# Kernel tuning notes

Hardware: AMD Instinct MI355X
Metric: run time of the kernel (lower is better)

The kernel has to match this reference:

```python
import jax, jax.numpy as jnp
import numpy as np

B, Q, C, H, W, CH = 16, 1024, 256, 32, 32, 8  # batch, queries, dim, grid, conv hidden


def setup_inputs() -> dict:
    key = jax.random.key(0)
    ks = jax.random.split(key, 8)
    return {
        "queries": jax.random.normal(ks[0], (B, Q, C), jnp.float32),
        "keys": jax.random.normal(ks[1], (B, H, W, C), jnp.float32),
        "pos": jax.random.randint(ks[2], (B, Q, 2), 0, H, dtype=jnp.int32),
        "rel_bias": jax.random.normal(ks[3], (2 * H - 1, 2 * W - 1), jnp.float32) * 0.02,
        "conv1_weight": jax.random.normal(ks[4], (CH, 1, 3, 3), jnp.float32) * 0.1,
        "conv1_bias": jnp.zeros((CH,), jnp.float32),
        "conv2_weight": jax.random.normal(ks[5], (1, CH, 3, 3), jnp.float32) * 0.1,
        "conv2_bias": jnp.zeros((1,), jnp.float32),
    }


def reference(queries, keys, pos, rel_bias, conv1_weight, conv1_bias, conv2_weight, conv2_bias):
    Bq, Qn, Cd = queries.shape
    _, Hh, Ww, _ = keys.shape
    # fused relative-grid attention scores: [B,Q,H,W]
    scores = jnp.einsum('bqc,bhwc->bqhw', queries, keys) / jnp.sqrt(jnp.float32(Cd))
    dh = jnp.arange(Hh)[None, None, :] - pos[..., 0][..., None] + (Hh - 1)  # [B,Q,H]
    dw = jnp.arange(Ww)[None, None, :] - pos[..., 1][..., None] + (Ww - 1)  # [B,Q,W]
    bias = rel_bias[dh[..., :, None], dw[..., None, :]]                     # [B,Q,H,W]
    attn = jax.nn.softmax((scores + bias).reshape(Bq, Qn, Hh * Ww), axis=-1)
    attn = attn.reshape(Bq, Qn, Hh, Ww)
    # residual conv block on each (1,H,W) attention map
    x = attn.reshape(Bq * Qn, 1, Hh, Ww)
    dn = ('NCHW', 'OIHW', 'NCHW')
    h = jax.lax.conv_general_dilated(x, conv1_weight, (1, 1), 'SAME', dimension_numbers=dn)
    h = jax.nn.relu(h + conv1_bias[None, :, None, None])
    h = jax.lax.conv_general_dilated(h, conv2_weight, (1, 1), 'SAME', dimension_numbers=dn)
    h = h + conv2_bias[None, :, None, None]
    return (x + h).reshape(Bq, Qn, Hh, Ww)
```

## Files before the change

kernel.cpp:

```cpp
#include <hip/hip_runtime.h>

typedef _Float16 h2 __attribute__((ext_vector_type(2)));
typedef _Float16 h8 __attribute__((ext_vector_type(8)));
typedef float f32x4 __attribute__((ext_vector_type(4)));

#define B_  16
#define Q_  1024
#define C_  256
#define HW_ 1024
#define TQA 32
#define NTA 512
#define QLD 264
#define BT  256
#define IPB 4
#define XRB 80
#define XIMGB (34 * XRB)
#define HRB 576

__device__ __forceinline__ h2 u2h(unsigned u) { return __builtin_bit_cast(h2, u); }
__device__ __forceinline__ unsigned h2u(h2 h) { return __builtin_bit_cast(unsigned, h); }

__device__ __forceinline__ float fdot2f(h2 a, h2 b, float c) {
#if __has_builtin(__builtin_amdgcn_fdot2)
    return __builtin_amdgcn_fdot2(a, b, c, false);
#else
    return c + (float)a[0] * (float)b[0] + (float)a[1] * (float)b[1];
#endif
}
__device__ __forceinline__ float dotw(unsigned x, unsigned w, float acc) {
    return fdot2f(u2h(x), u2h(w), acc);
}

__global__ void cvt_keys_f16(const float* __restrict__ src,
                             _Float16* __restrict__ dst, int n8) {
    int i = blockIdx.x * blockDim.x + threadIdx.x;
    if (i >= n8) return;
    const float4* s = (const float4*)src;
    float4 a = s[2 * i], b = s[2 * i + 1];
    h8 v;
    v[0] = (_Float16)a.x; v[1] = (_Float16)a.y; v[2] = (_Float16)a.z; v[3] = (_Float16)a.w;
    v[4] = (_Float16)b.x; v[5] = (_Float16)b.y; v[6] = (_Float16)b.z; v[7] = (_Float16)b.w;
    *(h8*)(dst + (size_t)i * 8) = v;
}

__global__ void pack_weights(const float* __restrict__ w1, const float* __restrict__ b1,
                             const float* __restrict__ w2, const float* __restrict__ b2,
                             unsigned* __restrict__ wpk) {
    int t = threadIdx.x;
    if (t < 24) {
        int ch = t / 3, dy = t - ch * 3;
        h2 v = {(_Float16)w1[ch * 9 + dy * 3 + 0], (_Float16)w1[ch * 9 + dy * 3 + 1]};
        wpk[t] = h2u(v);
    } else if (t < 48) {
        int i = t - 24; int ch = i / 3, dy = i - ch * 3;
        h2 v = {(_Float16)w1[ch * 9 + dy * 3 + 2], (_Float16)0.f};
        wpk[t] = h2u(v);
    } else if (t < 56) {
        wpk[t] = __builtin_bit_cast(unsigned, b1[t - 48]);
    } else if (t < 92) {
        int i = t - 56; int t9 = i >> 2, c2 = i & 3;
        h2 v = {(_Float16)w2[(2 * c2) * 9 + t9], (_Float16)w2[(2 * c2 + 1) * 9 + t9]};
        wpk[t] = h2u(v);
    } else if (t == 92) {
        wpk[t] = __builtin_bit_cast(unsigned, b2[0]);
    }
}

__global__ __launch_bounds__(NTA, 4) void attn_kernel(
    const float* __restrict__ queries, const _Float16* __restrict__ keysh,
    const int* __restrict__ pos, const float* __restrict__ rel_bias,
    _Float16* __restrict__ xmapg)
{
    __shared__ _Float16 q_lds[TQA * QLD];
    __shared__ _Float16 bias_lds[63 * 64];
    __shared__ float red_max[8][TQA];
    __shared__ float red_sum[8][TQA];
    __shared__ int2  pos_lds[TQA];

    const int tid = threadIdx.x;
    const int bid = blockIdx.x;
    const int swz = (bid & 7) * 64 + (bid >> 3);
    const int batch = swz >> 5;
    const int tile  = swz & 31;

    {
        const float4* qsrc = (const float4*)(queries + (size_t)(batch * Q_ + tile * TQA) * C_);
        #pragma unroll
        for (int i = 0; i < 4; ++i) {
            int e4 = i * NTA + tid;
            float4 v = qsrc[e4];
            int row = e4 >> 6, col4 = e4 & 63;
            _Float16* d = &q_lds[row * QLD + col4 * 4];
            d[0] = (_Float16)v.x; d[1] = (_Float16)v.y;
            d[2] = (_Float16)v.z; d[3] = (_Float16)v.w;
        }
        for (int idx = tid; idx < 63 * 63; idx += NTA) {
            int r = idx / 63;
            bias_lds[r * 64 + (idx - r * 63)] = (_Float16)rel_bias[idx];
        }
        if (tid < TQA)
            pos_lds[tid] = ((const int2*)pos)[batch * Q_ + tile * TQA + tid];
    }
    __syncthreads();

    const int lane = tid & 63;
    const int wv   = tid >> 6;
    const int kgrp = (lane >> 4) * 8;
    const int l15  = lane & 15;
    const int rowbase = (lane >> 4) << 2;

    f32x4 acc0[8], acc1[8];
    #pragma unroll
    for (int f = 0; f < 8; ++f) {
        acc0[f] = f32x4{0.f, 0.f, 0.f, 0.f};
        acc1[f] = f32x4{0.f, 0.f, 0.f, 0.f};
    }

    const _Float16* kb = keysh + (size_t)batch * (HW_ * C_)
                       + (size_t)(wv * 128 + l15) * C_ + kgrp;
    #pragma unroll
    for (int ks = 0; ks < 8; ++ks) {
        h8 a0 = *(const h8*)&q_lds[l15 * QLD + ks * 32 + kgrp];
        h8 a1 = *(const h8*)&q_lds[(16 + l15) * QLD + ks * 32 + kgrp];
        #pragma unroll
        for (int f = 0; f < 8; ++f) {
            h8 bfr = *(const h8*)(kb + f * (16 * C_) + ks * 32);
            acc0[f] = __builtin_amdgcn_mfma_f32_16x16x32_f16(a0, bfr, acc0[f], 0, 0, 0);
            acc1[f] = __builtin_amdgcn_mfma_f32_16x16x32_f16(a1, bfr, acc1[f], 0, 0, 0);
        }
    }

    int p0r[2][4], p1r[2][4];
    #pragma unroll
    for (int mt = 0; mt < 2; ++mt)
        #pragma unroll
        for (int r = 0; r < 4; ++r) {
            int2 pp = pos_lds[mt * 16 + rowbase + r];
            p0r[mt][r] = pp.x; p1r[mt][r] = pp.y;
        }

    float mrow[2][4];
    #pragma unroll
    for (int mt = 0; mt < 2; ++mt)
        #pragma unroll
        for (int r = 0; r < 4; ++r) mrow[mt][r] = -3e38f;

    #pragma unroll
    for (int f = 0; f < 8; ++f) {
        int col = wv * 128 + f * 16 + l15;
        int hh = col >> 5, ww = col & 31;
        #pragma unroll
        for (int r = 0; r < 4; ++r) {
            float s0 = acc0[f][r] * 0.0625f
                     + (float)bias_lds[(hh - p0r[0][r] + 31) * 64 + (ww - p1r[0][r] + 31)];
            acc0[f][r] = s0;
            mrow[0][r] = fmaxf(mrow[0][r], s0);
            float s1 = acc1[f][r] * 0.0625f
                     + (float)bias_lds[(hh - p0r[1][r] + 31) * 64 + (ww - p1r[1][r] + 31)];
            acc1[f][r] = s1;
            mrow[1][r] = fmaxf(mrow[1][r], s1);
        }
    }
    #pragma unroll
    for (int mt = 0; mt < 2; ++mt)
        #pragma unroll
        for (int r = 0; r < 4; ++r) {
            float m = mrow[mt][r];
            m = fmaxf(m, __shfl_xor(m, 1, 64));
            m = fmaxf(m, __shfl_xor(m, 2, 64));
            m = fmaxf(m, __shfl_xor(m, 4, 64));
            m = fmaxf(m, __shfl_xor(m, 8, 64));
            mrow[mt][r] = m;
        }
    if (l15 == 0) {
        #pragma unroll
        for (int mt = 0; mt < 2; ++mt)
            #pragma unroll
            for (int r = 0; r < 4; ++r)
                red_max[wv][mt * 16 + rowbase + r] = mrow[mt][r];
    }
    __syncthreads();

    float M4[2][4];
    #pragma unroll
    for (int mt = 0; mt < 2; ++mt)
        #pragma unroll
        for (int r = 0; r < 4; ++r) {
            float m = red_max[0][mt * 16 + rowbase + r];
            #pragma unroll
            for (int w = 1; w < 8; ++w) m = fmaxf(m, red_max[w][mt * 16 + rowbase + r]);
            M4[mt][r] = m;
        }

    float sm[2][4];
    #pragma unroll
    for (int mt = 0; mt < 2; ++mt)
        #pragma unroll
        for (int r = 0; r < 4; ++r) sm[mt][r] = 0.f;
    #pragma unroll
    for (int f = 0; f < 8; ++f) {
        #pragma unroll
        for (int r = 0; r < 4; ++r) {
            float e0 = __expf(acc0[f][r] - M4[0][r]);
            acc0[f][r] = e0; sm[0][r] += e0;
            float e1 = __expf(acc1[f][r] - M4[1][r]);
            acc1[f][r] = e1; sm[1][r] += e1;
        }
    }
    #pragma unroll
    for (int mt = 0; mt < 2; ++mt)
        #pragma unroll
        for (int r = 0; r < 4; ++r) {
            float s = sm[mt][r];
            s += __shfl_xor(s, 1, 64);
            s += __shfl_xor(s, 2, 64);
            s += __shfl_xor(s, 4, 64);
            s += __shfl_xor(s, 8, 64);
            sm[mt][r] = s;
        }
    if (l15 == 0) {
        #pragma unroll
        for (int mt = 0; mt < 2; ++mt)
            #pragma unroll
            for (int r = 0; r < 4; ++r)
                red_sum[wv][mt * 16 + rowbase + r] = sm[mt][r];
    }
    __syncthreads();

    float sinv[2][4];
    #pragma unroll
    for (int mt = 0; mt < 2; ++mt)
        #pragma unroll
        for (int r = 0; r < 4; ++r) {
            float S = red_sum[0][mt * 16 + rowbase + r];
            #pragma unroll
            for (int w = 1; w < 8; ++w) S += red_sum[w][mt * 16 + rowbase + r];
            sinv[mt][r] = 1.0f / S;
        }

    _Float16* xg = xmapg + (size_t)(batch * Q_ + tile * TQA) * HW_;
    #pragma unroll
    for (int f = 0; f < 8; ++f) {
        int col = wv * 128 + f * 16 + l15;
        #pragma unroll
        for (int r = 0; r < 4; ++r) {
            xg[(size_t)(rowbase + r) * HW_ + col] = (_Float16)(acc0[f][r] * sinv[0][r]);
            xg[(size_t)(16 + rowbase + r) * HW_ + col] = (_Float16)(acc1[f][r] * sinv[1][r]);
        }
    }
}

__global__ __launch_bounds__(BT, 4) void conv_kernel(
    const _Float16* __restrict__ xmapg, const unsigned* __restrict__ wpk,
    float* __restrict__ out)
{
    __shared__ __align__(16) char xall[16 + IPB * XIMGB];
    __shared__ __align__(16) char Hb[34 * HRB];
    __shared__ unsigned wsh[56];

    const int tid = threadIdx.x;
    const int bid = blockIdx.x;
    const int swz = (bid & 7) * 512 + (bid >> 3);
    const size_t img0 = (size_t)swz * IPB;

    {
        const uint4 z = uint4{0u, 0u, 0u, 0u};
        uint4* xz = (uint4*)xall;
        for (int i = tid; i < (int)sizeof(xall) / 16; i += BT) xz[i] = z;
        uint4* hz = (uint4*)Hb;
        for (int i = tid; i < (int)sizeof(Hb) / 16; i += BT) hz[i] = z;
    }
    if (tid < 56) wsh[tid] = wpk[tid];
    __syncthreads();

    #pragma unroll
    for (int i = 0; i < 2; ++i) {
        int c = i * BT + tid;
        int im = c >> 7, cc = c & 127, r = cc >> 2, q = cc & 3;
        uint4 v = *(const uint4*)(xmapg + img0 * HW_ + (size_t)im * HW_ + cc * 8);
        *(uint4*)(xall + 16 + im * XIMGB + (r + 1) * XRB + q * 16) = v;
    }

    unsigned wA[8][3], wB[8][3];
    float b1r[8];
    #pragma unroll
    for (int ch = 0; ch < 8; ++ch) {
        b1r[ch] = __builtin_bit_cast(float, wsh[48 + ch]);
        #pragma unroll
        for (int dy = 0; dy < 3; ++dy) {
            wA[ch][dy] = wsh[ch * 3 + dy];
            wB[ch][dy] = wsh[24 + ch * 3 + dy];
        }
    }
    unsigned w2s[9][4];
    #pragma unroll
    for (int t = 0; t < 9; ++t)
        #pragma unroll
        for (int c2 = 0; c2 < 4; ++c2) w2s[t][c2] = wpk[56 + t * 4 + c2];
    const float b2r = __builtin_bit_cast(float, wpk[92]);

    const int m4 = tid & 7;
    const int y  = tid >> 3;
    const int x0 = m4 << 2;

    const char* const xb  = xall + 16 + y * XRB + 2 * x0;
    char* const hwr = Hb + (y + 1) * HRB + m4 * 16;
    const char* const hrd = Hb + y * HRB + m4 * 16;

    __syncthreads();

    #pragma unroll 1
    for (int img = 0; img < IPB; ++img) {
        const char* xi = xb + img * XIMGB;

        unsigned Pm[3], Pc[3], Pe[3], A0[3], A1[3], E4[3];
        #pragma unroll
        for (int dy = 0; dy < 3; ++dy) {
            unsigned pv = *(const unsigned*)(xi + dy * XRB - 4);
            uint2 a01   = *(const uint2*)(xi + dy * XRB);
            unsigned e4 = *(const unsigned*)(xi + dy * XRB + 8);
            A0[dy] = a01.x; A1[dy] = a01.y; E4[dy] = e4;
            Pm[dy] = __builtin_amdgcn_alignbit(a01.x, pv, 16);
            Pc[dy] = __builtin_amdgcn_alignbit(a01.y, a01.x, 16);
            Pe[dy] = __builtin_amdgcn_alignbit(e4, a01.y, 16);
        }

        unsigned hvw[4][4];
        #pragma unroll
        for (int p = 0; p < 4; ++p) {
            const int cA = 2 * p, cB = 2 * p + 1;
            float sA[4], sB[4];
            #pragma unroll
            for (int j = 0; j < 4; ++j) { sA[j] = b1r[cA]; sB[j] = b1r[cB]; }
            #pragma unroll
            for (int dy = 0; dy < 3; ++dy) {
                sA[0] = dotw(Pm[dy], wA[cA][dy], sA[0]);
                sA[0] = dotw(Pc[dy], wB[cA][dy], sA[0]);
                sA[1] = dotw(A0[dy], wA[cA][dy], sA[1]);
                sA[1] = dotw(A1[dy], wB[cA][dy], sA[1]);
                sA[2] = dotw(Pc[dy], wA[cA][dy], sA[2]);
                sA[2] = dotw(Pe[dy], wB[cA][dy], sA[2]);
                sA[3] = dotw(A1[dy], wA[cA][dy], sA[3]);
                sA[3] = dotw(E4[dy], wB[cA][dy], sA[3]);
                sB[0] = dotw(Pm[dy], wA[cB][dy], sB[0]);
                sB[0] = dotw(Pc[dy], wB[cB][dy], sB[0]);
                sB[1] = dotw(A0[dy], wA[cB][dy], sB[1]);
                sB[1] = dotw(A1[dy], wB[cB][dy], sB[1]);
                sB[2] = dotw(Pc[dy], wA[cB][dy], sB[2]);
                sB[2] = dotw(Pe[dy], wB[cB][dy], sB[2]);
                sB[3] = dotw(A1[dy], wA[cB][dy], sB[3]);
                sB[3] = dotw(E4[dy], wB[cB][dy], sB[3]);
            }
            #pragma unroll
            for (int j = 0; j < 4; ++j) {
                h2 r;
                r[0] = (_Float16)fmaxf(sA[j], 0.f);
                r[1] = (_Float16)fmaxf(sB[j], 0.f);
                hvw[j][p] = h2u(r);
            }
        }

        __syncthreads();

        {
            *(uint4*)(hwr + 144) = uint4{hvw[0][0], hvw[0][1], hvw[0][2], hvw[0][3]};
            *(uint4*)(hwr + 288) = uint4{hvw[1][0], hvw[1][1], hvw[1][2], hvw[1][3]};
            *(uint4*)(hwr + 432) = uint4{hvw[2][0], hvw[2][1], hvw[2][2], hvw[2][3]};
            *(uint4*)(hwr + 16)  = uint4{hvw[3][0], hvw[3][1], hvw[3][2], hvw[3][3]};
        }
        __syncthreads();

        float a2[4] = {b2r, b2r, b2r, b2r};
        #pragma unroll
        for (int dy = 0; dy < 3; ++dy) {
            const char* rb = hrd + dy * HRB;
            uint4 Hv[6];
            Hv[0] = *(const uint4*)(rb + 0);
            Hv[1] = *(const uint4*)(rb + 144);
            Hv[2] = *(const uint4*)(rb + 288);
            Hv[3] = *(const uint4*)(rb + 432);
            Hv[4] = *(const uint4*)(rb + 16);
            Hv[5] = *(const uint4*)(rb + 160);
            #pragma unroll
            for (int j = 0; j < 4; ++j) {
                #pragma unroll
                for (int dx = 0; dx < 3; ++dx) {
                    const int tt = dy * 3 + dx;
                    const uint4 uu = Hv[j + dx];
                    a2[j] = dotw(uu.x, w2s[tt][0], a2[j]);
                    a2[j] = dotw(uu.y, w2s[tt][1], a2[j]);
                    a2[j] = dotw(uu.z, w2s[tt][2], a2[j]);
                    a2[j] = dotw(uu.w, w2s[tt][3], a2[j]);
                }
            }
        }
        {
            h2 lo = u2h(A0[1]), hi = u2h(A1[1]);
            float4 o;
            o.x = (float)lo[0] + a2[0];
            o.y = (float)lo[1] + a2[1];
            o.z = (float)hi[0] + a2[2];
            o.w = (float)hi[1] + a2[3];
            *(float4*)(out + (img0 + img) * HW_ + y * 32 + x0) = o;
        }
    }
}

extern "C" void kernel_launch(void* const* d_in, const int* in_sizes, int n_in,
                              void* d_out, int out_size, void* d_ws, size_t ws_size,
                              hipStream_t stream) {
    const float* queries  = (const float*)d_in[0];
    const float* keys     = (const float*)d_in[1];
    const int*   pos      = (const int*)d_in[2];
    const float* rel_bias = (const float*)d_in[3];
    const float* w1       = (const float*)d_in[4];
    const float* b1       = (const float*)d_in[5];
    const float* w2       = (const float*)d_in[6];
    const float* b2       = (const float*)d_in[7];
    float* out = (float*)d_out;

    unsigned*  wpk   = (unsigned*)d_ws;
    _Float16*  keysh = (_Float16*)((char*)d_ws + 4096);
    _Float16*  xmapg = (_Float16*)((char*)d_ws + 4096 + 8388608);

    const int n8 = (B_ * HW_ * C_) / 8;
    pack_weights<<<dim3(1), dim3(128), 0, stream>>>(w1, b1, w2, b2, wpk);
    cvt_keys_f16<<<dim3(n8 / 256), dim3(256), 0, stream>>>(keys, keysh, n8);
    attn_kernel<<<dim3(B_ * (Q_ / TQA)), dim3(NTA), 0, stream>>>(
        queries, keysh, pos, rel_bias, xmapg);
    conv_kernel<<<dim3((B_ * Q_) / IPB), dim3(BT), 0, stream>>>(xmapg, wpk, out);
}
```

Baseline: 115.8 us.

## Double query tile per attention block and drop padded LDS halos in conv kernel

The attention kernel now processes 64 queries per block instead of 32, with four M-tiles of accumulators. Each key fragment loaded from global memory therefore feeds four MFMAs instead of two, halving key traffic per query, at the cost of higher register pressure and lower occupancy (launch bounds go from 4 to 2). The conv kernel drops the zero-initialized padded halo buffers. It uses compact LDS rows, does boundary checks in registers, and stores the hidden activations in a swizzled layout, which removes the zero-fill pass and one barrier but adds branches and scalar halo loads.

```diff
diff --git a/kernel.cpp b/kernel.cpp
--- a/kernel.cpp
+++ b/kernel.cpp
@@ -8,14 +8,12 @@
 #define Q_  1024
 #define C_  256
 #define HW_ 1024
-#define TQA 32
+#define TQA 64
 #define NTA 512
 #define QLD 264
 #define BT  256
 #define IPB 4
-#define XRB 80
-#define XIMGB (34 * XRB)
-#define HRB 576
+#define XR  40
 
 __device__ __forceinline__ h2 u2h(unsigned u) { return __builtin_bit_cast(h2, u); }
 __device__ __forceinline__ unsigned h2u(h2 h) { return __builtin_bit_cast(unsigned, h); }
@@ -66,7 +64,7 @@
     }
 }
 
-__global__ __launch_bounds__(NTA, 4) void attn_kernel(
+__global__ __launch_bounds__(NTA, 2) void attn_kernel(
     const float* __restrict__ queries, const _Float16* __restrict__ keysh,
     const int* __restrict__ pos, const float* __restrict__ rel_bias,
     _Float16* __restrict__ xmapg)
@@ -79,14 +77,14 @@
 
     const int tid = threadIdx.x;
     const int bid = blockIdx.x;
-    const int swz = (bid & 7) * 64 + (bid >> 3);
-    const int batch = swz >> 5;
-    const int tile  = swz & 31;
+    const int swz = (bid & 7) * 32 + (bid >> 3);
+    const int batch = swz >> 4;
+    const int tile  = swz & 15;
 
     {
         const float4* qsrc = (const float4*)(queries + (size_t)(batch * Q_ + tile * TQA) * C_);
         #pragma unroll
-        for (int i = 0; i < 4; ++i) {
+        for (int i = 0; i < 8; ++i) {
             int e4 = i * NTA + tid;
             float4 v = qsrc[e4];
             int row = e4 >> 6, col4 = e4 & 63;
@@ -109,39 +107,41 @@
     const int l15  = lane & 15;
     const int rowbase = (lane >> 4) << 2;
 
-    f32x4 acc0[8], acc1[8];
-    #pragma unroll
-    for (int f = 0; f < 8; ++f) {
-        acc0[f] = f32x4{0.f, 0.f, 0.f, 0.f};
-        acc1[f] = f32x4{0.f, 0.f, 0.f, 0.f};
-    }
+    f32x4 acc[4][8];
+    #pragma unroll
+    for (int mt = 0; mt < 4; ++mt)
+        #pragma unroll
+        for (int f = 0; f < 8; ++f) acc[mt][f] = f32x4{0.f, 0.f, 0.f, 0.f};
 
     const _Float16* kb = keysh + (size_t)batch * (HW_ * C_)
                        + (size_t)(wv * 128 + l15) * C_ + kgrp;
     #pragma unroll
     for (int ks = 0; ks < 8; ++ks) {
-        h8 a0 = *(const h8*)&q_lds[l15 * QLD + ks * 32 + kgrp];
-        h8 a1 = *(const h8*)&q_lds[(16 + l15) * QLD + ks * 32 + kgrp];
+        h8 a[4];
+        #pragma unroll
+        for (int mt = 0; mt < 4; ++mt)
+            a[mt] = *(const h8*)&q_lds[(mt * 16 + l15) * QLD + ks * 32 + kgrp];
         #pragma unroll
         for (int f = 0; f < 8; ++f) {
             h8 bfr = *(const h8*)(kb + f * (16 * C_) + ks * 32);
-            acc0[f] = __builtin_amdgcn_mfma_f32_16x16x32_f16(a0, bfr, acc0[f], 0, 0, 0);
-            acc1[f] = __builtin_amdgcn_mfma_f32_16x16x32_f16(a1, bfr, acc1[f], 0, 0, 0);
-        }
-    }
-
-    int p0r[2][4], p1r[2][4];
-    #pragma unroll
-    for (int mt = 0; mt < 2; ++mt)
+            #pragma unroll
+            for (int mt = 0; mt < 4; ++mt)
+                acc[mt][f] = __builtin_amdgcn_mfma_f32_16x16x32_f16(a[mt], bfr, acc[mt][f], 0, 0, 0);
+        }
+    }
+
+    int p0r[4][4], p1r[4][4];
+    #pragma unroll
+    for (int mt = 0; mt < 4; ++mt)
         #pragma unroll
         for (int r = 0; r < 4; ++r) {
             int2 pp = pos_lds[mt * 16 + rowbase + r];
             p0r[mt][r] = pp.x; p1r[mt][r] = pp.y;
         }
 
-    float mrow[2][4];
-    #pragma unroll
-    for (int mt = 0; mt < 2; ++mt)
+    float mrow[4][4];
+    #pragma unroll
+    for (int mt = 0; mt < 4; ++mt)
         #pragma unroll
         for (int r = 0; r < 4; ++r) mrow[mt][r] = -3e38f;
 
@@ -150,19 +150,17 @@
         int col = wv * 128 + f * 16 + l15;
         int hh = col >> 5, ww = col & 31;
         #pragma unroll
-        for (int r = 0; r < 4; ++r) {
-            float s0 = acc0[f][r] * 0.0625f
-                     + (float)bias_lds[(hh - p0r[0][r] + 31) * 64 + (ww - p1r[0][r] + 31)];
-            acc0[f][r] = s0;
-            mrow[0][r] = fmaxf(mrow[0][r], s0);
-            float s1 = acc1[f][r] * 0.0625f
-                     + (float)bias_lds[(hh - p0r[1][r] + 31) * 64 + (ww - p1r[1][r] + 31)];
-            acc1[f][r] = s1;
-            mrow[1][r] = fmaxf(mrow[1][r], s1);
-        }
-    }
-    #pragma unroll
-    for (int mt = 0; mt < 2; ++mt)
+        for (int mt = 0; mt < 4; ++mt)
+            #pragma unroll
+            for (int r = 0; r < 4; ++r) {
+                float s = acc[mt][f][r] * 0.0625f
+                        + (float)bias_lds[(hh - p0r[mt][r] + 31) * 64 + (ww - p1r[mt][r] + 31)];
+                acc[mt][f][r] = s;
+                mrow[mt][r] = fmaxf(mrow[mt][r], s);
+            }
+    }
+    #pragma unroll
+    for (int mt = 0; mt < 4; ++mt)
         #pragma unroll
         for (int r = 0; r < 4; ++r) {
             float m = mrow[mt][r];
@@ -174,41 +172,38 @@
         }
     if (l15 == 0) {
         #pragma unroll
-        for (int mt = 0; mt < 2; ++mt)
+        for (int mt = 0; mt < 4; ++mt)
             #pragma unroll
             for (int r = 0; r < 4; ++r)
                 red_max[wv][mt * 16 + rowbase + r] = mrow[mt][r];
     }
     __syncthreads();
 
-    float M4[2][4];
-    #pragma unroll
-    for (int mt = 0; mt < 2; ++mt)
+    float sm[4][4];
+    #pragma unroll
+    for (int mt = 0; mt < 4; ++mt)
         #pragma unroll
         for (int r = 0; r < 4; ++r) {
             float m = red_max[0][mt * 16 + rowbase + r];
             #pragma unroll
             for (int w = 1; w < 8; ++w) m = fmaxf(m, red_max[w][mt * 16 + rowbase + r]);
-            M4[mt][r] = m;
-        }
-
-    float sm[2][4];
-    #pragma unroll
-    for (int mt = 0; mt < 2; ++mt)
-        #pragma unroll
-        for (int r = 0; r < 4; ++r) sm[mt][r] = 0.f;
+            mrow[mt][r] = m;
+            sm[mt][r] = 0.f;
+        }
+
     #pragma unroll
     for (int f = 0; f < 8; ++f) {
         #pragma unroll
-        for (int r = 0; r < 4; ++r) {
-            float e0 = __expf(acc0[f][r] - M4[0][r]);
-            acc0[f][r] = e0; sm[0][r] += e0;
-            float e1 = __expf(acc1[f][r] - M4[1][r]);
-            acc1[f][r] = e1; sm[1][r] += e1;
-        }
-    }
-    #pragma unroll
-    for (int mt = 0; mt < 2; ++mt)
+        for (int mt = 0; mt < 4; ++mt)
+            #pragma unroll
+            for (int r = 0; r < 4; ++r) {
+                float e = __expf(acc[mt][f][r] - mrow[mt][r]);
+                acc[mt][f][r] = e;
+                sm[mt][r] += e;
+            }
+    }
+    #pragma unroll
+    for (int mt = 0; mt < 4; ++mt)
         #pragma unroll
         for (int r = 0; r < 4; ++r) {
             float s = sm[mt][r];
@@ -220,32 +215,31 @@
         }
     if (l15 == 0) {
         #pragma unroll
-        for (int mt = 0; mt < 2; ++mt)
+        for (int mt = 0; mt < 4; ++mt)
             #pragma unroll
             for (int r = 0; r < 4; ++r)
                 red_sum[wv][mt * 16 + rowbase + r] = sm[mt][r];
     }
     __syncthreads();
 
-    float sinv[2][4];
-    #pragma unroll
-    for (int mt = 0; mt < 2; ++mt)
+    _Float16* xg = xmapg + (size_t)(batch * Q_ + tile * TQA) * HW_;
+    #pragma unroll
+    for (int mt = 0; mt < 4; ++mt) {
+        float sinv[4];
         #pragma unroll
         for (int r = 0; r < 4; ++r) {
             float S = red_sum[0][mt * 16 + rowbase + r];
             #pragma unroll
             for (int w = 1; w < 8; ++w) S += red_sum[w][mt * 16 + rowbase + r];
-            sinv[mt][r] = 1.0f / S;
-        }
-
-    _Float16* xg = xmapg + (size_t)(batch * Q_ + tile * TQA) * HW_;
-    #pragma unroll
-    for (int f = 0; f < 8; ++f) {
-        int col = wv * 128 + f * 16 + l15;
-        #pragma unroll
-        for (int r = 0; r < 4; ++r) {
-            xg[(size_t)(rowbase + r) * HW_ + col] = (_Float16)(acc0[f][r] * sinv[0][r]);
-            xg[(size_t)(16 + rowbase + r) * HW_ + col] = (_Float16)(acc1[f][r] * sinv[1][r]);
+            sinv[r] = 1.0f / S;
+        }
+        #pragma unroll
+        for (int f = 0; f < 8; ++f) {
+            int col = wv * 128 + f * 16 + l15;
+            #pragma unroll
+            for (int r = 0; r < 4; ++r)
+                xg[(size_t)(mt * 16 + rowbase + r) * HW_ + col]
+                    = (_Float16)(acc[mt][f][r] * sinv[r]);
         }
     }
 }
@@ -254,32 +248,24 @@
     const _Float16* __restrict__ xmapg, const unsigned* __restrict__ wpk,
     float* __restrict__ out)
 {
-    __shared__ __align__(16) char xall[16 + IPB * XIMGB];
-    __shared__ __align__(16) char Hb[34 * HRB];
-    __shared__ unsigned wsh[56];
+    __shared__ _Float16 ximg[IPB][32 * XR];
+    __shared__ __align__(16) char Hb[16384];
+    __shared__ unsigned wsh[96];
 
     const int tid = threadIdx.x;
     const int bid = blockIdx.x;
     const int swz = (bid & 7) * 512 + (bid >> 3);
     const size_t img0 = (size_t)swz * IPB;
 
-    {
-        const uint4 z = uint4{0u, 0u, 0u, 0u};
-        uint4* xz = (uint4*)xall;
-        for (int i = tid; i < (int)sizeof(xall) / 16; i += BT) xz[i] = z;
-        uint4* hz = (uint4*)Hb;
-        for (int i = tid; i < (int)sizeof(Hb) / 16; i += BT) hz[i] = z;
-    }
-    if (tid < 56) wsh[tid] = wpk[tid];
-    __syncthreads();
-
+    if (tid < 93) wsh[tid] = wpk[tid];
     #pragma unroll
     for (int i = 0; i < 2; ++i) {
         int c = i * BT + tid;
-        int im = c >> 7, cc = c & 127, r = cc >> 2, q = cc & 3;
+        int im = c >> 7, cc = c & 127;
         uint4 v = *(const uint4*)(xmapg + img0 * HW_ + (size_t)im * HW_ + cc * 8);
-        *(uint4*)(xall + 16 + im * XIMGB + (r + 1) * XRB + q * 16) = v;
-    }
+        *(uint4*)&ximg[im][(cc >> 2) * XR + (cc & 3) * 8] = v;
+    }
+    __syncthreads();
 
     unsigned wA[8][3], wB[8][3];
     float b1r[8];
@@ -296,33 +282,34 @@
     #pragma unroll
     for (int t = 0; t < 9; ++t)
         #pragma unroll
-        for (int c2 = 0; c2 < 4; ++c2) w2s[t][c2] = wpk[56 + t * 4 + c2];
-    const float b2r = __builtin_bit_cast(float, wpk[92]);
-
-    const int m4 = tid & 7;
+        for (int c2 = 0; c2 < 4; ++c2) w2s[t][c2] = wsh[56 + t * 4 + c2];
+    const float b2r = __builtin_bit_cast(float, wsh[92]);
+
+    const int x0 = (tid & 7) << 2;
     const int y  = tid >> 3;
-    const int x0 = m4 << 2;
-
-    const char* const xb  = xall + 16 + y * XRB + 2 * x0;
-    char* const hwr = Hb + (y + 1) * HRB + m4 * 16;
-    const char* const hrd = Hb + y * HRB + m4 * 16;
-
-    __syncthreads();
 
     #pragma unroll 1
     for (int img = 0; img < IPB; ++img) {
-        const char* xi = xb + img * XIMGB;
-
-        unsigned Pm[3], Pc[3], Pe[3], A0[3], A1[3], E4[3];
+        const _Float16* xim = &ximg[img][0];
+
+        unsigned Pm[3], A0[3], Pc[3], A1[3], Pe[3], E4[3];
         #pragma unroll
         for (int dy = 0; dy < 3; ++dy) {
-            unsigned pv = *(const unsigned*)(xi + dy * XRB - 4);
-            uint2 a01   = *(const uint2*)(xi + dy * XRB);
-            unsigned e4 = *(const unsigned*)(xi + dy * XRB + 8);
-            A0[dy] = a01.x; A1[dy] = a01.y; E4[dy] = e4;
-            Pm[dy] = __builtin_amdgcn_alignbit(a01.x, pv, 16);
-            Pc[dy] = __builtin_amdgcn_alignbit(a01.y, a01.x, 16);
-            Pe[dy] = __builtin_amdgcn_alignbit(e4, a01.y, 16);
+            int yy = y + dy - 1;
+            unsigned b0 = 0, b1v = 0, em = 0, e4 = 0;
+            if ((unsigned)yy < 32u) {
+                const _Float16* row = xim + yy * XR + x0;
+                uint2 bb = *(const uint2*)row;
+                b0 = bb.x; b1v = bb.y;
+                if (x0 > 0)      em = *(const unsigned short*)(row - 1);
+                if (x0 + 4 < 32) e4 = *(const unsigned short*)(row + 4);
+            }
+            Pm[dy] = (em & 0xffffu) | (b0 << 16);
+            A0[dy] = b0;
+            Pc[dy] = (b0 >> 16) | (b1v << 16);
+            A1[dy] = b1v;
+            Pe[dy] = (b1v >> 16) | (e4 << 16);
+            E4[dy] = e4;
         }
 
         unsigned hvw[4][4];
@@ -363,24 +350,36 @@
         __syncthreads();
 
         {
-            *(uint4*)(hwr + 144) = uint4{hvw[0][0], hvw[0][1], hvw[0][2], hvw[0][3]};
-            *(uint4*)(hwr + 288) = uint4{hvw[1][0], hvw[1][1], hvw[1][2], hvw[1][3]};
-            *(uint4*)(hwr + 432) = uint4{hvw[2][0], hvw[2][1], hvw[2][2], hvw[2][3]};
-            *(uint4*)(hwr + 16)  = uint4{hvw[3][0], hvw[3][1], hvw[3][2], hvw[3][3]};
+            char* wbp = Hb + (y << 9);
+            const int m4 = x0 >> 2;
+            #pragma unroll
+            for (int j = 0; j < 4; ++j) {
+                uint4 hv = {hvw[j][0], hvw[j][1], hvw[j][2], hvw[j][3]};
+                *(uint4*)(wbp + ((j * 8 + m4) << 4)) = hv;
+            }
         }
         __syncthreads();
 
         float a2[4] = {b2r, b2r, b2r, b2r};
         #pragma unroll
         for (int dy = 0; dy < 3; ++dy) {
-            const char* rb = hrd + dy * HRB;
+            int yy = y + dy - 1;
             uint4 Hv[6];
-            Hv[0] = *(const uint4*)(rb + 0);
-            Hv[1] = *(const uint4*)(rb + 144);
-            Hv[2] = *(const uint4*)(rb + 288);
-            Hv[3] = *(const uint4*)(rb + 432);
-            Hv[4] = *(const uint4*)(rb + 16);
-            Hv[5] = *(const uint4*)(rb + 160);
+            if ((unsigned)yy < 32u) {
+                const char* rb = Hb + (yy << 9);
+                #pragma unroll
+                for (int k = 0; k < 6; ++k) {
+                    int c = x0 - 1 + k;
+                    if ((unsigned)c < 32u) {
+                        unsigned g = (((unsigned)(c & 3)) << 3) | ((unsigned)c >> 2);
+                        Hv[k] = *(const uint4*)(rb + (g << 4));
+                    } else
+                        Hv[k] = uint4{0u, 0u, 0u, 0u};
+                }
+            } else {
+                #pragma unroll
+                for (int k = 0; k < 6; ++k) Hv[k] = uint4{0u, 0u, 0u, 0u};
+            }
             #pragma unroll
             for (int j = 0; j < 4; ++j) {
                 #pragma unroll
@@ -395,7 +394,9 @@
             }
         }
         {
-            h2 lo = u2h(A0[1]), hi = u2h(A1[1]);
+            const _Float16* xr4 = xim + y * XR + x0;
+            uint2 rr = *(const uint2*)xr4;
+            h2 lo = u2h(rr.x), hi = u2h(rr.y);
             float4 o;
             o.x = (float)lo[0] + a2[0];
             o.y = (float)lo[1] + a2[1];
```

Result: slower. 215.6 us (+86.2%).
